# Kernel optimization log

Hardware: AMD Instinct MI355X
Metric: run time of the kernel (lower is better)

## Reference

```python
import jax, jax.numpy as jnp
import numpy as np

FORGET_BIAS = 1.0  # tf.nn.rnn_cell.LSTMCell default
HIDDEN = 64


def setup_inputs() -> dict:
    key = jax.random.key(0)
    k1, k2 = jax.random.split(key)
    B, T, D = 4096, 9, 512
    x = jax.random.normal(k1, (B, T, D), dtype=jnp.float32)
    # Fused LSTM kernel: [(D + H), 4H], gate order (i, j, f, o) as in TF LSTMCell
    kernel = jax.random.normal(k2, (D + HIDDEN, 4 * HIDDEN), dtype=jnp.float32) * 0.02
    bias = jnp.zeros((4 * HIDDEN,), dtype=jnp.float32)
    return {"x": x, "kernel": kernel, "bias": bias}


def _lstm_scan(x, kernel, bias):
    B, T, D = x.shape
    H = HIDDEN
    # Split kernel into input and recurrent parts for a cleaner scan body.
    Wx = kernel[:D]          # [D, 4H]
    Wh = kernel[D:]          # [H, 4H]
    # Precompute input contributions for all timesteps in one big GEMM.
    xg = jnp.einsum('btd,dg->btg', x, Wx) + bias  # [B, T, 4H]

    def step(carry, xg_t):
        c, h = carry
        gates = xg_t + h @ Wh  # [B, 4H]
        i, j, f, o = jnp.split(gates, 4, axis=-1)  # TF gate order: i, j, f, o
        c_new = jax.nn.sigmoid(f + FORGET_BIAS) * c + jax.nn.sigmoid(i) * jnp.tanh(j)
        h_new = jax.nn.sigmoid(o) * jnp.tanh(c_new)
        return (c_new, h_new), h_new

    c0 = jnp.zeros((B, H), dtype=x.dtype)
    h0 = jnp.zeros((B, H), dtype=x.dtype)
    _, hs = jax.lax.scan(step, (c0, h0), jnp.swapaxes(xg, 0, 1))  # hs: [T, B, H]
    return jnp.transpose(hs, (1, 0, 2))  # [B, T, H]


def reference(x, kernel, bias):
    return _lstm_scan(x, kernel, bias)
```

## Files before the change

kernel.cpp:

```cpp
#include <hip/hip_runtime.h>
#include <math.h>

#define T_STEPS 9
#define D_IN    512
#define HID     64
#define G4      256
#define BPB     8
#define MTP     80

typedef short  short8 __attribute__((ext_vector_type(8)));
typedef float  f32x4  __attribute__((ext_vector_type(4)));
typedef unsigned int uint;
typedef unsigned short ushort;

__device__ __forceinline__ ushort f2bf(float f) {
    uint u = __float_as_uint(f);
    u = (u + 0x7FFFu + ((u >> 16) & 1u)) >> 16;
    return (ushort)u;
}
__device__ __forceinline__ float fsig(float x) {
    return 1.0f / (1.0f + __expf(-x));
}
__device__ __forceinline__ float ftanh(float x) {
    float t = __expf(-2.0f * fabsf(x));
    float r = (1.0f - t) / (1.0f + t);
    return copysignf(r, x);
}

__global__ __launch_bounds__(256)
void prep_w(const float* __restrict__ kern, ushort* __restrict__ wxT,
            ushort* __restrict__ whT)
{
    int i = blockIdx.x * 256 + threadIdx.x;
    if (i < 131072) {
        int j  = i & 7;
        int n  = (i >> 3) & 255;
        int qk = (i >> 11) & 3;
        int k0 = i >> 13;
        int k  = k0 * 32 + qk * 8 + j;
        wxT[i] = f2bf(kern[(size_t)k * G4 + n]);
    } else {
        int i2 = i - 131072;
        int j  = i2 & 7;
        int n  = (i2 >> 3) & 255;
        int kq = i2 >> 11;
        whT[i2] = f2bf(kern[(size_t)(D_IN + kq * 8 + j) * G4 + n]);
    }
}

__global__ __launch_bounds__(256, 2)
void lstm_fused(const float* __restrict__ x, const ushort* __restrict__ wxT,
                const ushort* __restrict__ whT, const float* __restrict__ bias,
                float* __restrict__ out)
{
    __shared__ ushort sA[4 * MTP * 8];
    __shared__ ushort sH[8 * 16 * 8];

    const int t = threadIdx.x;
    const int w = t >> 6, l = t & 63;
    const int lane15 = l & 15, quad = l >> 4;
    const int u = w * 16 + lane15;

    short8 whF[4][2];
    #pragma unroll
    for (int g = 0; g < 4; ++g)
        #pragma unroll
        for (int kh = 0; kh < 2; ++kh)
            whF[g][kh] = *(const short8*)&whT[(size_t)((kh * 4 + quad) * 256 + g * 64 + u) * 8];

    ((uint2*)sH)[t] = (uint2){0u, 0u};

    const float* xblk = x + (size_t)blockIdx.x * (BPB * T_STEPS) * D_IN;
    const int mhalf = t >> 1, kh_a = t & 1;
    const bool ld = (mhalf < BPB * T_STEPS);
    const bool zr = (!ld && mhalf < MTP);
    const int b_ = mhalf & 7, s_ = mhalf >> 3;
    const float* pA = xblk + (size_t)(b_ * T_STEPS + s_) * D_IN + kh_a * 16;

    float4 rA[4];
    if (ld) {
        #pragma unroll
        for (int q = 0; q < 4; ++q) rA[q] = ((const float4*)pA)[q];
    }

    f32x4 acc[5][4];
    #pragma unroll
    for (int i = 0; i < 5; ++i)
        #pragma unroll
        for (int g = 0; g < 4; ++g)
            acc[i][g] = (f32x4){0.f, 0.f, 0.f, 0.f};

    for (int k0 = 0; k0 < 16; ++k0) {
        __syncthreads();
        if (ld) {
            uint4 lo, hi;
            lo.x = f2bf(rA[0].x) | ((uint)f2bf(rA[0].y) << 16);
            lo.y = f2bf(rA[0].z) | ((uint)f2bf(rA[0].w) << 16);
            lo.z = f2bf(rA[1].x) | ((uint)f2bf(rA[1].y) << 16);
            lo.w = f2bf(rA[1].z) | ((uint)f2bf(rA[1].w) << 16);
            hi.x = f2bf(rA[2].x) | ((uint)f2bf(rA[2].y) << 16);
            hi.y = f2bf(rA[2].z) | ((uint)f2bf(rA[2].w) << 16);
            hi.z = f2bf(rA[3].x) | ((uint)f2bf(rA[3].y) << 16);
            hi.w = f2bf(rA[3].z) | ((uint)f2bf(rA[3].w) << 16);
            *(uint4*)&sA[((kh_a * 2 + 0) * MTP + mhalf) * 8] = lo;
            *(uint4*)&sA[((kh_a * 2 + 1) * MTP + mhalf) * 8] = hi;
        } else if (zr) {
            uint4 z = {0u, 0u, 0u, 0u};
            *(uint4*)&sA[((kh_a * 2 + 0) * MTP + mhalf) * 8] = z;
            *(uint4*)&sA[((kh_a * 2 + 1) * MTP + mhalf) * 8] = z;
        }
        __syncthreads();

        if (ld && k0 < 15) {
            const float4* nA = (const float4*)(pA + (k0 + 1) * 32);
            #pragma unroll
            for (int q = 0; q < 4; ++q) rA[q] = nA[q];
        }

        const ushort* wxc = wxT + (size_t)(k0 * 4 + quad) * 256 * 8;
        short8 bF[4];
        #pragma unroll
        for (int g = 0; g < 4; ++g)
            bF[g] = *(const short8*)&wxc[(size_t)(g * 64 + u) * 8];

        #pragma unroll
        for (int i = 0; i < 5; ++i) {
            short8 aF = *(const short8*)&sA[(quad * MTP + i * 16 + lane15) * 8];
            #pragma unroll
            for (int g = 0; g < 4; ++g)
                acc[i][g] = __builtin_amdgcn_mfma_f32_16x16x32_bf16(aF, bF[g], acc[i][g], 0, 0, 0);
        }
    }

    float bia[4];
    bia[0] = bias[u];
    bia[1] = bias[64 + u];
    bia[2] = bias[128 + u] + 1.0f;
    bia[3] = bias[192 + u];

    float cst[4] = {0.f, 0.f, 0.f, 0.f};
    const int b0 = blockIdx.x * BPB;

    #pragma unroll
    for (int s = 0; s < T_STEPS; ++s) {
        const int  i = s >> 1;
        const int  p = s & 1;
        const bool active = ((quad >> 1) == p);
        const int  bofs = (quad & 1) * 4;

        f32x4 g4[4];
        #pragma unroll
        for (int g = 0; g < 4; ++g)
            #pragma unroll
            for (int r = 0; r < 4; ++r)
                g4[g][r] = acc[i][g][r] + bia[g];

        short8 aF[2];
        #pragma unroll
        for (int kh = 0; kh < 2; ++kh)
            aF[kh] = *(const short8*)&sH[((kh * 4 + quad) * 16 + lane15) * 8];

        #pragma unroll
        for (int g = 0; g < 4; ++g)
            #pragma unroll
            for (int kh = 0; kh < 2; ++kh)
                g4[g] = __builtin_amdgcn_mfma_f32_16x16x32_bf16(aF[kh], whF[g][kh], g4[g], 0, 0, 0);

        __syncthreads();

        const int wrow = 8 * ((s + 1) & 1);
        #pragma unroll
        for (int r = 0; r < 4; ++r) {
            float cp = __shfl_xor(cst[r], 32);
            if (active) {
                float ii = fsig(g4[0][r]);
                float jj = ftanh(g4[1][r]);
                float ff = fsig(g4[2][r]);
                float oo = fsig(g4[3][r]);
                float c  = ff * cp + ii * jj;
                cst[r] = c;
                float h = oo * ftanh(c);
                int bb = bofs + r;
                out[((size_t)(b0 + bb) * T_STEPS + s) * HID + u] = h;
                sH[((u >> 3) * 16 + wrow + bb) * 8 + (u & 7)] = f2bf(h);
            }
        }
        __syncthreads();
    }
}

extern "C" void kernel_launch(void* const* d_in, const int* in_sizes, int n_in,
                              void* d_out, int out_size, void* d_ws, size_t ws_size,
                              hipStream_t stream)
{
    const float* x    = (const float*)d_in[0];
    const float* kern = (const float*)d_in[1];
    const float* bias = (const float*)d_in[2];
    float* out = (float*)d_out;

    const int B = in_sizes[0] / (T_STEPS * D_IN);

    ushort* wxT = (ushort*)d_ws;
    ushort* whT = (ushort*)((char*)d_ws + 262144);

    prep_w<<<576, 256, 0, stream>>>(kern, wxT, whT);
    lstm_fused<<<B / BPB, 256, 0, stream>>>(x, wxT, whT, bias, out);
}
```

Baseline: 135.4 us.

## Double-buffer input GEMM staging with register prefetch and swizzled LDS

Restructures the input-projection GEMM loop to use two LDS buffers with one barrier per k-step, prefetching x two steps ahead in registers and Wx fragments one step ahead. It also applies an XOR swizzle to the LDS row index to reduce bank conflicts, and reassigns loader threads so only 36 lanes per wave load. The aim is to hide global-load latency behind MFMA work and remove a barrier per iteration, in exchange for more register pressure from the extra prefetch buffers and the fully unrolled loop.

```diff
diff --git a/kernel.cpp b/kernel.cpp
--- a/kernel.cpp
+++ b/kernel.cpp
@@ -25,6 +25,9 @@
     float t = __expf(-2.0f * fabsf(x));
     float r = (1.0f - t) / (1.0f + t);
     return copysignf(r, x);
+}
+__device__ __forceinline__ int saidx(int qk, int row) {
+    return (qk * MTP + (row ^ ((row >> 3) & 7))) * 8;
 }
 
 __global__ __launch_bounds__(256)
@@ -53,7 +56,7 @@
                 const ushort* __restrict__ whT, const float* __restrict__ bias,
                 float* __restrict__ out)
 {
-    __shared__ ushort sA[4 * MTP * 8];
+    __shared__ ushort sA[2][4 * MTP * 8];
     __shared__ ushort sH[8 * 16 * 8];
 
     const int t = threadIdx.x;
@@ -61,76 +64,106 @@
     const int lane15 = l & 15, quad = l >> 4;
     const int u = w * 16 + lane15;
 
+    const bool isld = (l < 36);
+    const int lrow = 2 * l + (w >> 1);
+    const int lkh  = w & 1;
+    const int lb = lrow & 7, ls = lrow >> 3;
+    const float* xblk = x + (size_t)blockIdx.x * (BPB * T_STEPS) * D_IN;
+    const float* pA = xblk + (size_t)(lb * T_STEPS + ls) * D_IN + lkh * 16;
+
+    float4 r0[4], ra[2][4];
+    if (isld) {
+        #pragma unroll
+        for (int q = 0; q < 4; ++q) r0[q]    = ((const float4*)pA)[q];
+        #pragma unroll
+        for (int q = 0; q < 4; ++q) ra[1][q] = ((const float4*)(pA + 32))[q];
+        #pragma unroll
+        for (int q = 0; q < 4; ++q) ra[0][q] = ((const float4*)(pA + 64))[q];
+    }
+    if (t < 64) {
+        int buf = t >> 5, slot = t & 31;
+        int qk = slot >> 3, row = 72 + (slot & 7);
+        uint4 z = {0u, 0u, 0u, 0u};
+        *(uint4*)&sA[buf][(qk * MTP + row) * 8] = z;
+    }
+    ((uint2*)sH)[t] = (uint2){0u, 0u};
+
+    if (isld) {
+        uint4 lo, hi;
+        lo.x = f2bf(r0[0].x) | ((uint)f2bf(r0[0].y) << 16);
+        lo.y = f2bf(r0[0].z) | ((uint)f2bf(r0[0].w) << 16);
+        lo.z = f2bf(r0[1].x) | ((uint)f2bf(r0[1].y) << 16);
+        lo.w = f2bf(r0[1].z) | ((uint)f2bf(r0[1].w) << 16);
+        hi.x = f2bf(r0[2].x) | ((uint)f2bf(r0[2].y) << 16);
+        hi.y = f2bf(r0[2].z) | ((uint)f2bf(r0[2].w) << 16);
+        hi.z = f2bf(r0[3].x) | ((uint)f2bf(r0[3].y) << 16);
+        hi.w = f2bf(r0[3].z) | ((uint)f2bf(r0[3].w) << 16);
+        *(uint4*)&sA[0][saidx(lkh * 2 + 0, lrow)] = lo;
+        *(uint4*)&sA[0][saidx(lkh * 2 + 1, lrow)] = hi;
+    }
+
+    short8 bFb[2][4];
+    {
+        const ushort* wxc = wxT + (size_t)(0 * 4 + quad) * 256 * 8;
+        #pragma unroll
+        for (int g = 0; g < 4; ++g)
+            bFb[0][g] = *(const short8*)&wxc[(size_t)(g * 64 + u) * 8];
+    }
+
+    f32x4 acc[5][4];
+    #pragma unroll
+    for (int i = 0; i < 5; ++i)
+        #pragma unroll
+        for (int g = 0; g < 4; ++g)
+            acc[i][g] = (f32x4){0.f, 0.f, 0.f, 0.f};
+
+    #pragma unroll
+    for (int k = 0; k < 16; ++k) {
+        __syncthreads();
+
+        if (k < 15) {
+            const ushort* wxc = wxT + (size_t)((k + 1) * 4 + quad) * 256 * 8;
+            #pragma unroll
+            for (int g = 0; g < 4; ++g)
+                bFb[(k + 1) & 1][g] = *(const short8*)&wxc[(size_t)(g * 64 + u) * 8];
+        }
+
+        #pragma unroll
+        for (int i = 0; i < 5; ++i) {
+            short8 aF = *(const short8*)&sA[k & 1][saidx(quad, i * 16 + lane15)];
+            #pragma unroll
+            for (int g = 0; g < 4; ++g)
+                acc[i][g] = __builtin_amdgcn_mfma_f32_16x16x32_bf16(aF, bFb[k & 1][g], acc[i][g], 0, 0, 0);
+        }
+
+        if (k < 15 && isld) {
+            float4 v0 = ra[(k + 1) & 1][0], v1 = ra[(k + 1) & 1][1];
+            float4 v2 = ra[(k + 1) & 1][2], v3 = ra[(k + 1) & 1][3];
+            uint4 lo, hi;
+            lo.x = f2bf(v0.x) | ((uint)f2bf(v0.y) << 16);
+            lo.y = f2bf(v0.z) | ((uint)f2bf(v0.w) << 16);
+            lo.z = f2bf(v1.x) | ((uint)f2bf(v1.y) << 16);
+            lo.w = f2bf(v1.z) | ((uint)f2bf(v1.w) << 16);
+            hi.x = f2bf(v2.x) | ((uint)f2bf(v2.y) << 16);
+            hi.y = f2bf(v2.z) | ((uint)f2bf(v2.w) << 16);
+            hi.z = f2bf(v3.x) | ((uint)f2bf(v3.y) << 16);
+            hi.w = f2bf(v3.z) | ((uint)f2bf(v3.w) << 16);
+            *(uint4*)&sA[(k + 1) & 1][saidx(lkh * 2 + 0, lrow)] = lo;
+            *(uint4*)&sA[(k + 1) & 1][saidx(lkh * 2 + 1, lrow)] = hi;
+            if (k < 13) {
+                const float4* np = (const float4*)(pA + (k + 3) * 32);
+                #pragma unroll
+                for (int q = 0; q < 4; ++q) ra[(k + 1) & 1][q] = np[q];
+            }
+        }
+    }
+
     short8 whF[4][2];
     #pragma unroll
     for (int g = 0; g < 4; ++g)
         #pragma unroll
         for (int kh = 0; kh < 2; ++kh)
             whF[g][kh] = *(const short8*)&whT[(size_t)((kh * 4 + quad) * 256 + g * 64 + u) * 8];
-
-    ((uint2*)sH)[t] = (uint2){0u, 0u};
-
-    const float* xblk = x + (size_t)blockIdx.x * (BPB * T_STEPS) * D_IN;
-    const int mhalf = t >> 1, kh_a = t & 1;
-    const bool ld = (mhalf < BPB * T_STEPS);
-    const bool zr = (!ld && mhalf < MTP);
-    const int b_ = mhalf & 7, s_ = mhalf >> 3;
-    const float* pA = xblk + (size_t)(b_ * T_STEPS + s_) * D_IN + kh_a * 16;
-
-    float4 rA[4];
-    if (ld) {
-        #pragma unroll
-        for (int q = 0; q < 4; ++q) rA[q] = ((const float4*)pA)[q];
-    }
-
-    f32x4 acc[5][4];
-    #pragma unroll
-    for (int i = 0; i < 5; ++i)
-        #pragma unroll
-        for (int g = 0; g < 4; ++g)
-            acc[i][g] = (f32x4){0.f, 0.f, 0.f, 0.f};
-
-    for (int k0 = 0; k0 < 16; ++k0) {
-        __syncthreads();
-        if (ld) {
-            uint4 lo, hi;
-            lo.x = f2bf(rA[0].x) | ((uint)f2bf(rA[0].y) << 16);
-            lo.y = f2bf(rA[0].z) | ((uint)f2bf(rA[0].w) << 16);
-            lo.z = f2bf(rA[1].x) | ((uint)f2bf(rA[1].y) << 16);
-            lo.w = f2bf(rA[1].z) | ((uint)f2bf(rA[1].w) << 16);
-            hi.x = f2bf(rA[2].x) | ((uint)f2bf(rA[2].y) << 16);
-            hi.y = f2bf(rA[2].z) | ((uint)f2bf(rA[2].w) << 16);
-            hi.z = f2bf(rA[3].x) | ((uint)f2bf(rA[3].y) << 16);
-            hi.w = f2bf(rA[3].z) | ((uint)f2bf(rA[3].w) << 16);
-            *(uint4*)&sA[((kh_a * 2 + 0) * MTP + mhalf) * 8] = lo;
-            *(uint4*)&sA[((kh_a * 2 + 1) * MTP + mhalf) * 8] = hi;
-        } else if (zr) {
-            uint4 z = {0u, 0u, 0u, 0u};
-            *(uint4*)&sA[((kh_a * 2 + 0) * MTP + mhalf) * 8] = z;
-            *(uint4*)&sA[((kh_a * 2 + 1) * MTP + mhalf) * 8] = z;
-        }
-        __syncthreads();
-
-        if (ld && k0 < 15) {
-            const float4* nA = (const float4*)(pA + (k0 + 1) * 32);
-            #pragma unroll
-            for (int q = 0; q < 4; ++q) rA[q] = nA[q];
-        }
-
-        const ushort* wxc = wxT + (size_t)(k0 * 4 + quad) * 256 * 8;
-        short8 bF[4];
-        #pragma unroll
-        for (int g = 0; g < 4; ++g)
-            bF[g] = *(const short8*)&wxc[(size_t)(g * 64 + u) * 8];
-
-        #pragma unroll
-        for (int i = 0; i < 5; ++i) {
-            short8 aF = *(const short8*)&sA[(quad * MTP + i * 16 + lane15) * 8];
-            #pragma unroll
-            for (int g = 0; g < 4; ++g)
-                acc[i][g] = __builtin_amdgcn_mfma_f32_16x16x32_bf16(aF, bF[g], acc[i][g], 0, 0, 0);
-        }
-    }
 
     float bia[4];
     bia[0] = bias[u];
```

Result: no change. 134.7 us (-0.5%).

## Stage whole x tile in LDS with swizzle, drop per-k barriers, double-buffer Wx

Applied to the files above, without the earlier changes.

The block's full 72x512 input tile is now loaded up front with coalesced float4 reads, converted to bf16 and stored in a large XOR-swizzled LDS buffer. The K loop then runs fully unrolled with no barriers, and Wx fragments are prefetched one step ahead into a double buffer. The aim is to remove 32 per-K __syncthreads and the serialized global-load/convert pipeline. In exchange the kernel uses about 80KB of LDS per block, which may cut occupancy below the 2 blocks per CU the launch bounds request. It also holds many registers live during the bulk load.

```diff
diff --git a/kernel.cpp b/kernel.cpp
--- a/kernel.cpp
+++ b/kernel.cpp
@@ -6,7 +6,7 @@
 #define HID     64
 #define G4      256
 #define BPB     8
-#define MTP     80
+#define ROWS    72
 
 typedef short  short8 __attribute__((ext_vector_type(8)));
 typedef float  f32x4  __attribute__((ext_vector_type(4)));
@@ -53,84 +53,84 @@
                 const ushort* __restrict__ whT, const float* __restrict__ bias,
                 float* __restrict__ out)
 {
-    __shared__ ushort sA[4 * MTP * 8];
-    __shared__ ushort sH[8 * 16 * 8];
+    __shared__ ushort sAm[80 * 512];
+    ushort* const sH = &sAm[72 * 512];
 
     const int t = threadIdx.x;
     const int w = t >> 6, l = t & 63;
     const int lane15 = l & 15, quad = l >> 4;
     const int u = w * 16 + lane15;
 
+    {
+        uint4 z = {0u, 0u, 0u, 0u};
+        ((uint4*)&sAm[72 * 512])[t]       = z;
+        ((uint4*)&sAm[72 * 512])[t + 256] = z;
+    }
+
+    short8 bFb[2][4];
+    {
+        const ushort* wxc = wxT + (size_t)(0 * 4 + quad) * 256 * 8;
+        #pragma unroll
+        for (int g = 0; g < 4; ++g)
+            bFb[0][g] = *(const short8*)&wxc[(size_t)(g * 64 + u) * 8];
+    }
+
+    const float4* xblk = (const float4*)(x + (size_t)blockIdx.x * (ROWS * D_IN));
+    #pragma unroll
+    for (int h = 0; h < 2; ++h) {
+        float4 v[18];
+        #pragma unroll
+        for (int q = 0; q < 18; ++q)
+            v[q] = xblk[(h * 18 + q) * 256 + t];
+        #pragma unroll
+        for (int q = 0; q < 18; ++q) {
+            int flat = (h * 18 + q) * 256 + t;
+            int r    = flat >> 7;
+            int colq = flat & 127;
+            int b = r / 9, s = r - b * 9;
+            int row = s * 8 + b;
+            int kq  = colq >> 1;
+            int adr = row * 512 + ((kq ^ (row & 7)) << 3) + ((colq & 1) << 2);
+            uint2 p;
+            p.x = f2bf(v[q].x) | ((uint)f2bf(v[q].y) << 16);
+            p.y = f2bf(v[q].z) | ((uint)f2bf(v[q].w) << 16);
+            *(uint2*)&sAm[adr] = p;
+        }
+    }
+    __syncthreads();
+
+    f32x4 acc[5][4];
+    #pragma unroll
+    for (int i = 0; i < 5; ++i)
+        #pragma unroll
+        for (int g = 0; g < 4; ++g)
+            acc[i][g] = (f32x4){0.f, 0.f, 0.f, 0.f};
+
+    #pragma unroll
+    for (int k = 0; k < 16; ++k) {
+        if (k < 15) {
+            const ushort* wxc = wxT + (size_t)((k + 1) * 4 + quad) * 256 * 8;
+            #pragma unroll
+            for (int g = 0; g < 4; ++g)
+                bFb[(k + 1) & 1][g] = *(const short8*)&wxc[(size_t)(g * 64 + u) * 8];
+        }
+        #pragma unroll
+        for (int i = 0; i < 5; ++i) {
+            int row = i * 16 + lane15;
+            short8 aF = *(const short8*)
+                &sAm[row * 512 + (((k * 4 + quad) ^ (row & 7)) << 3)];
+            #pragma unroll
+            for (int g = 0; g < 4; ++g)
+                acc[i][g] = __builtin_amdgcn_mfma_f32_16x16x32_bf16(aF, bFb[k & 1][g], acc[i][g], 0, 0, 0);
+        }
+    }
+
     short8 whF[4][2];
     #pragma unroll
     for (int g = 0; g < 4; ++g)
         #pragma unroll
         for (int kh = 0; kh < 2; ++kh)
             whF[g][kh] = *(const short8*)&whT[(size_t)((kh * 4 + quad) * 256 + g * 64 + u) * 8];
-
-    ((uint2*)sH)[t] = (uint2){0u, 0u};
-
-    const float* xblk = x + (size_t)blockIdx.x * (BPB * T_STEPS) * D_IN;
-    const int mhalf = t >> 1, kh_a = t & 1;
-    const bool ld = (mhalf < BPB * T_STEPS);
-    const bool zr = (!ld && mhalf < MTP);
-    const int b_ = mhalf & 7, s_ = mhalf >> 3;
-    const float* pA = xblk + (size_t)(b_ * T_STEPS + s_) * D_IN + kh_a * 16;
-
-    float4 rA[4];
-    if (ld) {
-        #pragma unroll
-        for (int q = 0; q < 4; ++q) rA[q] = ((const float4*)pA)[q];
-    }
-
-    f32x4 acc[5][4];
-    #pragma unroll
-    for (int i = 0; i < 5; ++i)
-        #pragma unroll
-        for (int g = 0; g < 4; ++g)
-            acc[i][g] = (f32x4){0.f, 0.f, 0.f, 0.f};
-
-    for (int k0 = 0; k0 < 16; ++k0) {
-        __syncthreads();
-        if (ld) {
-            uint4 lo, hi;
-            lo.x = f2bf(rA[0].x) | ((uint)f2bf(rA[0].y) << 16);
-            lo.y = f2bf(rA[0].z) | ((uint)f2bf(rA[0].w) << 16);
-            lo.z = f2bf(rA[1].x) | ((uint)f2bf(rA[1].y) << 16);
-            lo.w = f2bf(rA[1].z) | ((uint)f2bf(rA[1].w) << 16);
-            hi.x = f2bf(rA[2].x) | ((uint)f2bf(rA[2].y) << 16);
-            hi.y = f2bf(rA[2].z) | ((uint)f2bf(rA[2].w) << 16);
-            hi.z = f2bf(rA[3].x) | ((uint)f2bf(rA[3].y) << 16);
-            hi.w = f2bf(rA[3].z) | ((uint)f2bf(rA[3].w) << 16);
-            *(uint4*)&sA[((kh_a * 2 + 0) * MTP + mhalf) * 8] = lo;
-            *(uint4*)&sA[((kh_a * 2 + 1) * MTP + mhalf) * 8] = hi;
-        } else if (zr) {
-            uint4 z = {0u, 0u, 0u, 0u};
-            *(uint4*)&sA[((kh_a * 2 + 0) * MTP + mhalf) * 8] = z;
-            *(uint4*)&sA[((kh_a * 2 + 1) * MTP + mhalf) * 8] = z;
-        }
-        __syncthreads();
-
-        if (ld && k0 < 15) {
-            const float4* nA = (const float4*)(pA + (k0 + 1) * 32);
-            #pragma unroll
-            for (int q = 0; q < 4; ++q) rA[q] = nA[q];
-        }
-
-        const ushort* wxc = wxT + (size_t)(k0 * 4 + quad) * 256 * 8;
-        short8 bF[4];
-        #pragma unroll
-        for (int g = 0; g < 4; ++g)
-            bF[g] = *(const short8*)&wxc[(size_t)(g * 64 + u) * 8];
-
-        #pragma unroll
-        for (int i = 0; i < 5; ++i) {
-            short8 aF = *(const short8*)&sA[(quad * MTP + i * 16 + lane15) * 8];
-            #pragma unroll
-            for (int g = 0; g < 4; ++g)
-                acc[i][g] = __builtin_amdgcn_mfma_f32_16x16x32_bf16(aF, bF[g], acc[i][g], 0, 0, 0);
-        }
-    }
 
     float bia[4];
     bia[0] = bias[u];
```

Result: faster. 127.9 us (-5.5%).
